# Kernel tuning notes

Hardware: AMD Instinct MI355X
Metric: run time of the kernel (lower is better)

Reference implementation:

```python
import jax, jax.numpy as jnp
from jax import lax
import numpy as np

H, W, C = 128, 128, 1024          # backbone feature map (stride-16, ResNet C4)
STRIDE = 16
NUM_ANCHORS = 9                   # 3 scales x 3 ratios
IOU_THRESHOLD = 0.7
SCORE_THRESHOLD = 0.5


def _make_anchors():
    scales = np.array([128.0, 256.0, 512.0], np.float32)
    ratios = np.array([0.5, 1.0, 2.0], np.float32)
    hs = (scales[:, None] * np.sqrt(ratios)[None, :]).reshape(-1)   # [9]
    ws = (scales[:, None] / np.sqrt(ratios)[None, :]).reshape(-1)   # [9]
    cy = (np.arange(H, dtype=np.float32) + 0.5) * STRIDE
    cx = (np.arange(W, dtype=np.float32) + 0.5) * STRIDE
    anc = np.zeros((H, W, NUM_ANCHORS, 4), np.float32)
    anc[..., 0] = cy[:, None, None]
    anc[..., 1] = cx[None, :, None]
    anc[..., 2] = hs
    anc[..., 3] = ws
    return anc.reshape(-1, 4)      # [N,4] as (cy, cx, h, w)


def _conv(x, w, b):
    return lax.conv_general_dilated(
        x, w, (1, 1), 'SAME', dimension_numbers=('NHWC', 'HWIO', 'NHWC')) + b


def _rpn_head(features, w1, b1, w2, b2, w_score, b_score, w_box, b_box):
    x = jax.nn.relu(features)
    x = _conv(x, w1, b1)
    x = jax.nn.relu(x)
    x = _conv(x, w2, b2)
    scores = jax.nn.sigmoid(_conv(x, w_score, b_score))   # [1,H,W,9]
    shifts = _conv(x, w_box, b_box)                        # [1,H,W,36]
    return scores.reshape(-1, 1), shifts.reshape(-1, 4)


def _decode(shifts, anchors):
    acy, acx, ah, aw = anchors[:, 0], anchors[:, 1], anchors[:, 2], anchors[:, 3]
    dy, dx, dh, dw = shifts[:, 0], shifts[:, 1], shifts[:, 2], shifts[:, 3]
    cy = acy + dy * ah
    cx = acx + dx * aw
    h = ah * jnp.exp(dh)
    w = aw * jnp.exp(dw)
    y1 = jnp.clip(cy - 0.5 * h, 0.0, H * STRIDE)
    x1 = jnp.clip(cx - 0.5 * w, 0.0, W * STRIDE)
    y2 = jnp.clip(cy + 0.5 * h, 0.0, H * STRIDE)
    x2 = jnp.clip(cx + 0.5 * w, 0.0, W * STRIDE)
    return jnp.stack([y1, x1, y2, x2], axis=-1)            # [N,4]


def _nms(boxes, scores, max_out):
    """Greedy NMS like tf.image.non_max_suppression, fixed-size padded output."""
    n = boxes.shape[0]
    areas = (boxes[:, 2] - boxes[:, 0]) * (boxes[:, 3] - boxes[:, 1])

    def body(state):
        suppressed, sel, count = state
        masked = jnp.where(suppressed, -jnp.inf, scores)
        i = jnp.argmax(masked)
        valid = masked[i] >= SCORE_THRESHOLD
        sel = sel.at[count].set(jnp.where(valid, i.astype(jnp.int32), -1))
        count = count + valid.astype(jnp.int32)
        b = boxes[i]
        iy = jnp.maximum(0.0, jnp.minimum(b[2], boxes[:, 2]) - jnp.maximum(b[0], boxes[:, 0]))
        ix = jnp.maximum(0.0, jnp.minimum(b[3], boxes[:, 3]) - jnp.maximum(b[1], boxes[:, 1]))
        inter = iy * ix
        iou = inter / (areas[i] + areas - inter + 1e-9)
        new_sup = (suppressed | (iou > IOU_THRESHOLD)).at[i].set(True)
        suppressed = jnp.where(valid, new_sup, jnp.ones_like(suppressed))
        return suppressed, sel, count

    def cond(state):
        suppressed, sel, count = state
        return (count < max_out) & (~jnp.all(suppressed))

    sel0 = jnp.full((max_out,), -1, jnp.int32)
    sup0 = jnp.zeros((n,), bool)
    _, sel, _ = lax.while_loop(cond, body, (sup0, sel0, jnp.int32(0)))
    valid = sel >= 0
    idx = jnp.where(valid, sel, 0)
    return boxes[idx] * valid[:, None], scores[idx] * valid, valid


def setup_inputs() -> dict:
    key = jax.random.key(0)
    ks = jax.random.split(key, 5)
    def init_w(k, shape, fan_in, scale=1.0):
        return jax.random.normal(k, shape, jnp.float32) * (scale / np.sqrt(fan_in))
    features = jax.random.normal(ks[0], (1, H, W, C), jnp.float32)
    w1 = init_w(ks[1], (3, 3, C, 512), 9 * C)
    b1 = jnp.zeros((512,), jnp.float32)
    w2 = init_w(ks[2], (3, 3, 512, 512), 9 * 512)
    b2 = jnp.zeros((512,), jnp.float32)
    w_score = init_w(ks[3], (1, 1, 512, NUM_ANCHORS), 512)
    b_score = jnp.zeros((NUM_ANCHORS,), jnp.float32)
    w_box = init_w(ks[4], (1, 1, 512, 4 * NUM_ANCHORS), 512, scale=0.1)
    b_box = jnp.zeros((4 * NUM_ANCHORS,), jnp.float32)
    return {"features": features, "w1": w1, "b1": b1, "w2": w2, "b2": b2,
            "w_score": w_score, "b_score": b_score,
            "w_box": w_box, "b_box": b_box, "region_limit": 300}


def reference(features, w1, b1, w2, b2, w_score, b_score, w_box, b_box, region_limit):
    pred_scores, pred_shifts = _rpn_head(features, w1, b1, w2, b2,
                                         w_score, b_score, w_box, b_box)
    anchors = jnp.asarray(_make_anchors())
    boxes = _decode(pred_shifts, anchors)
    return _nms(boxes, pred_scores[:, 0], int(region_limit))
```

## Files before the change

kernel.cpp:

```cpp
#include <hip/hip_runtime.h>

#define HW 128
#define COUTC 512
#define NB 4097
#define NSEL 300
#define T_TOP 4096
#define TW 64
#define FAST_N 1024

typedef _Float16 half8 __attribute__((ext_vector_type(8)));
typedef _Float16 half4v __attribute__((ext_vector_type(4)));
typedef float floatx4 __attribute__((ext_vector_type(4)));

#define NWS_A1H   ((size_t)0)
#define NWS_A1L   ((size_t)34611200)
#define NWS_W1H   ((size_t)69222400)
#define NWS_W1L   ((size_t)78659584)
#define NWS_A2H   ((size_t)88096768)
#define NWS_A2L   ((size_t)105402368)
#define NWS_W2H   ((size_t)122707968)
#define NWS_W2L   ((size_t)127426560)
#define NWS_X2    ((size_t)132145152)
#define NWS_BOXES ((size_t)165699584)
#define NWS_KEYS  ((size_t)168058880)
#define NWS_SKEYS ((size_t)169238528)
#define NWS_HIST  ((size_t)170418176)
#define NWS_CUR   ((size_t)170434816)
#define NWS_CNT   ((size_t)170451456)
#define NWS_BASE  ((size_t)170451712)
#define NWS_TOTAL ((size_t)170468352)

#define WS_X1     ((size_t)0)
#define WS_X2     ((size_t)33554432)
#define WS_BOXES  ((size_t)67108864)
#define WS_KEYS   ((size_t)69468160)
#define WS_SKEYS  ((size_t)70647808)
#define WS_HIST   ((size_t)71827456)
#define WS_CUR    ((size_t)71844096)
#define WS_CNT    ((size_t)71860736)
#define WS_BASE   ((size_t)71860992)

__device__ __forceinline__ void glds16(const void* g, void* l) {
    __builtin_amdgcn_global_load_lds(
        (const __attribute__((address_space(1))) void*)g,
        (__attribute__((address_space(3))) void*)l, 16, 0, 0);
}


__global__ __launch_bounds__(256) void convert_feat_kernel(
    const float* __restrict__ feat, _Float16* __restrict__ ah, _Float16* __restrict__ al)
{
    __shared__ __align__(16) _Float16 lh[130 * 32];
    __shared__ __align__(16) _Float16 ll[130 * 32];
    int pr = blockIdx.x;
    int chunk = blockIdx.y;
    int t = threadIdx.x;
    int c  = t & 31;
    int pg = t >> 5;
    bool interior = (pr >= 1 && pr <= 128);
    if (interior) {
        for (int px = pg; px < 128; px += 8) {
            float x = feat[((size_t)(pr - 1) * 128 + px) * 1024 + chunk * 32 + c];
            x = fmaxf(x, 0.f);
            _Float16 hi = (_Float16)x;
            lh[(px + 1) * 32 + c] = hi;
            ll[(px + 1) * 32 + c] = (_Float16)(x - (float)hi);
        }
    } else {
        for (int px = pg; px < 128; px += 8) {
            lh[(px + 1) * 32 + c] = (_Float16)0.f;
            ll[(px + 1) * 32 + c] = (_Float16)0.f;
        }
    }
    if (t < 32) {
        lh[t] = (_Float16)0.f;          ll[t] = (_Float16)0.f;
        lh[129 * 32 + t] = (_Float16)0.f; ll[129 * 32 + t] = (_Float16)0.f;
    }
    __syncthreads();
    size_t base = (size_t)pr * 133120 + (size_t)chunk * 4160;
    for (int i = t; i < 520; i += 256) {
        int sub = i / 130;
        int pc  = i - sub * 130;
        *(float4*)&ah[base + sub * 1040 + pc * 8] = *(const float4*)&lh[pc * 32 + sub * 8];
        *(float4*)&al[base + sub * 1040 + pc * 8] = *(const float4*)&ll[pc * 32 + sub * 8];
    }
}

template<int CIN>
__device__ __forceinline__ void convert_w_body(
    int b, const float* __restrict__ w, _Float16* __restrict__ wh, _Float16* __restrict__ wl)
{
    constexpr int NU = CIN / 8;
    int gid = b * 256 + threadIdx.x;
    int oc = gid & 511;
    int rest = gid >> 9;
    int u = rest & (NU - 1);
    int tap = rest / NU;
    if (tap >= 9) return;
    int k0 = u * 8;
    half8 vh, vl;
    #pragma unroll
    for (int j = 0; j < 8; ++j) {
        float v = w[((size_t)tap * CIN + k0 + j) * 512 + oc] * 64.f;
        _Float16 hi = (_Float16)v;
        vh[j] = hi;
        vl[j] = (_Float16)(v - (float)hi);
    }
    size_t o = (size_t)tap * CIN * 512 + (size_t)(k0 >> 5) * 16384
             + (size_t)((k0 >> 3) & 3) * 4096 + (size_t)oc * 8;
    *(half8*)(wh + o) = vh;
    *(half8*)(wl + o) = vl;
}

__global__ __launch_bounds__(256) void prep_kernel(
    const float* __restrict__ w1, _Float16* __restrict__ w1h, _Float16* __restrict__ w1l,
    const float* __restrict__ w2, _Float16* __restrict__ w2h, _Float16* __restrict__ w2l,
    const float* __restrict__ w_s, const float* __restrict__ w_b,
    _Float16* __restrict__ wbh, _Float16* __restrict__ wbl,
    _Float16* __restrict__ a2h, _Float16* __restrict__ a2l)
{
    int b = blockIdx.x;
    if (b < 2304) { convert_w_body<1024>(b, w1, w1h, w1l); return; }
    if (b < 3456) { convert_w_body<512>(b - 2304, w2, w2h, w2l); return; }
    if (b < 3584) {
        int gid = (b - 3456) * 256 + threadIdx.x;
        int n = gid & 63;
        int k = gid >> 6;
        float v = 0.f;
        if (n < 9)       v = w_s[k * 9 + n] * 64.f;
        else if (n < 45) v = w_b[k * 36 + (n - 9)] * 64.f;
        _Float16 hi = (_Float16)v;
        size_t o = (size_t)(k >> 5) * 2048 + (size_t)((k >> 3) & 3) * 512 + (size_t)n * 8 + (k & 7);
        wbh[o] = hi;
        wbl[o] = (_Float16)(v - (float)hi);
        return;
    }
    {
        int i = b - 3584;
        int pr, pc;
        if (i < 130)      { pr = 0;        pc = i; }
        else if (i < 260) { pr = 129;      pc = i - 130; }
        else if (i < 388) { pr = i - 259;  pc = 0; }
        else              { pr = i - 387;  pc = 129; }
        int t = threadIdx.x;
        if (t >= 128) return;
        _Float16* dst = (t & 64) ? a2l : a2h;
        int u = t & 63;
        size_t o = (size_t)pr * 66560 + (size_t)(u >> 2) * 4160 + (size_t)(u & 3) * 1040 + (size_t)pc * 8;
        *(float4*)(dst + o) = make_float4(0.f, 0.f, 0.f, 0.f);
    }
}

template<int CIN, bool PAD>
__global__ __launch_bounds__(256) void conv_mfma_kernel(
    const _Float16* __restrict__ ah, const _Float16* __restrict__ al,
    const _Float16* __restrict__ wh, const _Float16* __restrict__ wl,
    const float* __restrict__ bias,
    _Float16* __restrict__ oh, _Float16* __restrict__ ol)
{
    constexpr int ROWSTR = CIN * 130;
    constexpr int TAPW   = CIN * 512;
    __shared__ __align__(16) _Float16 lds[12288];

    int bx = blockIdx.x;
    int h  = bx & 127;
    int n0 = (bx >> 7) << 6;

    int tid  = threadIdx.x;
    int wave = tid >> 6;
    int lane = tid & 63;
    int fr = lane & 15;
    int fq = lane >> 4;

    int aoff0 = fq * 1040 + (32 * wave + fr) * 8;
    int aoff1 = aoff0 + 128;
    int boffB = fq * 4096 + (n0 + 32 * (wave & 1) + 16 * (wave >> 1) + fr) * 8;

    int wm = wave & 1, wn = wave >> 1;

    floatx4 acc[4][2];
    #pragma unroll
    for (int i = 0; i < 4; ++i)
        #pragma unroll
        for (int j = 0; j < 2; ++j)
            acc[i][j] = (floatx4){0.f, 0.f, 0.f, 0.f};

    _Float16* A0 = lds + wave * 1024;
    _Float16* L0 = lds + 4096 + wave * 1024;
    _Float16* B0 = lds + 8192 + (wave & 1) * 1024 + (wave >> 1) * 512;
    _Float16* C0 = B0 + 2048;

    const _Float16* rAh = lds + wm * 2048 + fq * 128 + fr * 8;
    const _Float16* rAl = rAh + 4096;
    const _Float16* rBh = lds + 8192 + wn * 1024 + fq * 128 + fr * 8;
    const _Float16* rBl = rBh + 2048;

    #pragma unroll
    for (int tap = 0; tap < 9; ++tap) {
        int dy = tap / 3 - 1, dx = tap % 3 - 1;
        const _Float16* gAh = ah + (size_t)(h + dy + 1) * ROWSTR + (dx + 1) * 8;
        const _Float16* gAl = al + (size_t)(h + dy + 1) * ROWSTR + (dx + 1) * 8;
        const _Float16* gBh = wh + (size_t)tap * TAPW;
        const _Float16* gBl = wl + (size_t)tap * TAPW;

        for (int kc = 0; kc < CIN; kc += 32) {
            int ab = (kc >> 5) * 4160;
            int bb = (kc >> 5) * 16384;
            glds16(gAh + ab + aoff0, A0);
            glds16(gAh + ab + aoff1, A0 + 512);
            glds16(gAl + ab + aoff0, L0);
            glds16(gAl + ab + aoff1, L0 + 512);
            glds16(gBh + bb + boffB, B0);
            glds16(gBl + bb + boffB, C0);
            __syncthreads();

            half8 fah[4], fal[4], fbh[2], fbl[2];
            #pragma unroll
            for (int i = 0; i < 4; ++i) {
                fah[i] = *(const half8*)(rAh + i * 512);
                fal[i] = *(const half8*)(rAl + i * 512);
            }
            #pragma unroll
            for (int j = 0; j < 2; ++j) {
                fbh[j] = *(const half8*)(rBh + j * 512);
                fbl[j] = *(const half8*)(rBl + j * 512);
            }
            #pragma unroll
            for (int i = 0; i < 4; ++i)
                #pragma unroll
                for (int j = 0; j < 2; ++j)
                    acc[i][j] = __builtin_amdgcn_mfma_f32_16x16x32_f16(fah[i], fbh[j], acc[i][j], 0, 0, 0);
            #pragma unroll
            for (int i = 0; i < 4; ++i)
                #pragma unroll
                for (int j = 0; j < 2; ++j)
                    acc[i][j] = __builtin_amdgcn_mfma_f32_16x16x32_f16(fah[i], fbl[j], acc[i][j], 0, 0, 0);
            #pragma unroll
            for (int i = 0; i < 4; ++i)
                #pragma unroll
                for (int j = 0; j < 2; ++j)
                    acc[i][j] = __builtin_amdgcn_mfma_f32_16x16x32_f16(fal[i], fbh[j], acc[i][j], 0, 0, 0);
            __syncthreads();
        }
    }

    const float scale = 1.f / 64.f;
    int em = 64 * wm + fq * 4;
    int en = 32 * wn + fr;
    #pragma unroll
    for (int j = 0; j < 2; ++j) {
        int oc = n0 + en + 16 * j;
        float b2 = bias[oc];
        #pragma unroll
        for (int i = 0; i < 4; ++i) {
            #pragma unroll
            for (int r = 0; r < 4; ++r) {
                int w = em + 16 * i + r;
                float v = fmaf(acc[i][j][r], scale, b2);
                if (PAD) {
                    v = fmaxf(v, 0.f);
                    _Float16 hi = (_Float16)v;
                    size_t o = (size_t)(h + 1) * 66560 + (size_t)(oc >> 5) * 4160
                             + (size_t)((oc >> 3) & 3) * 1040 + (size_t)(w + 1) * 8 + (oc & 7);
                    oh[o] = hi;
                    ol[o] = (_Float16)(v - (float)hi);
                } else {
                    _Float16 hi = (_Float16)v;
                    size_t o = (size_t)h * 65536 + (size_t)(oc >> 5) * 4096
                             + (size_t)((oc >> 3) & 3) * 1024 + (size_t)w * 8 + (oc & 7);
                    oh[o] = hi;
                    ol[o] = (_Float16)(v - (float)hi);
                }
            }
        }
    }
}

__device__ __forceinline__ void decode_emit(
    int gi, float z, float dyv, float dxv, float dhv, float dwv,
    float4* __restrict__ boxes, unsigned long long* __restrict__ keys,
    int* __restrict__ cnt, int* __restrict__ hist)
{
    int a = gi % 9;
    int pix = gi / 9;
    int h = pix >> 7, w = pix & 127;
    float sc  = (a < 3) ? 128.f : ((a < 6) ? 256.f : 512.f);
    int r = a - (a / 3) * 3;
    float ratio = (r == 0) ? 0.5f : ((r == 1) ? 1.f : 2.f);
    float sr = sqrtf(ratio);
    float ahh = sc * sr, aww = sc / sr;
    float acy = ((float)h + 0.5f) * 16.f;
    float acx = ((float)w + 0.5f) * 16.f;
    float cy = fmaf(dyv, ahh, acy);
    float cx = fmaf(dxv, aww, acx);
    float hh = ahh * expf(dhv);
    float ww = aww * expf(dwv);
    float y1 = fminf(fmaxf(cy - 0.5f * hh, 0.f), 2048.f);
    float x1 = fminf(fmaxf(cx - 0.5f * ww, 0.f), 2048.f);
    float y2 = fminf(fmaxf(cy + 0.5f * hh, 0.f), 2048.f);
    float x2 = fminf(fmaxf(cx + 0.5f * ww, 0.f), 2048.f);
    boxes[gi] = make_float4(y1, x1, y2, x2);
    float s = 1.f / (1.f + expf(-z));
    if (s >= 0.5f) {
        unsigned u = __float_as_uint(s);
        unsigned d = 0x3F800000u - u;
        unsigned long long key = ((unsigned long long)d << 18) | (unsigned)gi;
        int p = atomicAdd(cnt, 1);
        keys[p] = key;
        atomicAdd(&hist[d >> 11], 1);
    }
}

__global__ __launch_bounds__(256) void heads_mfma_kernel(
    const _Float16* __restrict__ xh, const _Float16* __restrict__ xl,
    const _Float16* __restrict__ wbh, const _Float16* __restrict__ wbl,
    const float* __restrict__ b_s, const float* __restrict__ b_b,
    float4* __restrict__ boxes, unsigned long long* __restrict__ keys,
    int* __restrict__ cnt, int* __restrict__ hist)
{
    __shared__ __align__(16) char smem[24576];
    _Float16* sAh = (_Float16*)smem;
    _Float16* sAl = (_Float16*)(smem + 8192);
    _Float16* sBh = (_Float16*)(smem + 16384);
    _Float16* sBl = (_Float16*)(smem + 20480);
    float* outs = (float*)smem;
    __shared__ float sb[48];

    int tid  = threadIdx.x;
    int wave = tid >> 6;
    int lane = tid & 63;
    int fr = lane & 15;
    int fq = lane >> 4;
    if (tid < 48) sb[tid] = (tid < 9) ? b_s[tid] : ((tid < 45) ? b_b[tid - 9] : 0.f);

    int h = blockIdx.x;
    int wm = wave & 1, wn = wave >> 1;

    floatx4 acc[4][2];
    #pragma unroll
    for (int i = 0; i < 4; ++i)
        #pragma unroll
        for (int j = 0; j < 2; ++j)
            acc[i][j] = (floatx4){0.f, 0.f, 0.f, 0.f};

    for (int kc = 0; kc < 16; ++kc) {
        const _Float16* gxh = xh + (size_t)h * 65536 + kc * 4096;
        const _Float16* gxl = xl + (size_t)h * 65536 + kc * 4096;
        glds16(gxh + tid * 8,        sAh + tid * 8);
        glds16(gxh + 2048 + tid * 8, sAh + 2048 + tid * 8);
        glds16(gxl + tid * 8,        sAl + tid * 8);
        glds16(gxl + 2048 + tid * 8, sAl + 2048 + tid * 8);
        glds16(wbh + kc * 2048 + tid * 8, sBh + tid * 8);
        glds16(wbl + kc * 2048 + tid * 8, sBl + tid * 8);
        __syncthreads();

        half8 fah[4], fal[4], fbh[2], fbl[2];
        #pragma unroll
        for (int i = 0; i < 4; ++i) {
            int px = wm * 64 + 16 * i + fr;
            int aaddr = fq * 1024 + px * 8;
            fah[i] = *(const half8*)(sAh + aaddr);
            fal[i] = *(const half8*)(sAl + aaddr);
        }
        #pragma unroll
        for (int j = 0; j < 2; ++j) {
            int n = wn * 32 + 16 * j + fr;
            int baddr = fq * 512 + n * 8;
            fbh[j] = *(const half8*)(sBh + baddr);
            fbl[j] = *(const half8*)(sBl + baddr);
        }
        #pragma unroll
        for (int i = 0; i < 4; ++i)
            #pragma unroll
            for (int j = 0; j < 2; ++j) {
                acc[i][j] = __builtin_amdgcn_mfma_f32_16x16x32_f16(fah[i], fbh[j], acc[i][j], 0, 0, 0);
                acc[i][j] = __builtin_amdgcn_mfma_f32_16x16x32_f16(fah[i], fbl[j], acc[i][j], 0, 0, 0);
                acc[i][j] = __builtin_amdgcn_mfma_f32_16x16x32_f16(fal[i], fbh[j], acc[i][j], 0, 0, 0);
            }
        __syncthreads();
    }

    const float scale = 1.f / 64.f;
    #pragma unroll
    for (int i = 0; i < 4; ++i)
        #pragma unroll
        for (int j = 0; j < 2; ++j)
            #pragma unroll
            for (int r = 0; r < 4; ++r) {
                int px = wm * 64 + 16 * i + fq * 4 + r;
                int n = wn * 32 + 16 * j + fr;
                if (n < 48)
                    outs[px * 48 + n] = fmaf(acc[i][j][r], scale, sb[n]);
            }
    __syncthreads();

    if (tid < 128) {
        int p = tid;
        #pragma unroll
        for (int a = 0; a < 9; ++a) {
            float z   = outs[p * 48 + a];
            float dyv = outs[p * 48 + 9 + 4 * a + 0];
            float dxv = outs[p * 48 + 9 + 4 * a + 1];
            float dhv = outs[p * 48 + 9 + 4 * a + 2];
            float dwv = outs[p * 48 + 9 + 4 * a + 3];
            int gi = (h * 128 + p) * 9 + a;
            decode_emit(gi, z, dyv, dxv, dhv, dwv, boxes, keys, cnt, hist);
        }
    }
}

template<int CIN, bool RELU_IN, bool RELU_OUT>
__global__ __launch_bounds__(256) void conv3x3_kernel(
    const float* __restrict__ in, const float* __restrict__ wgt,
    const float* __restrict__ bias, float* __restrict__ out)
{
    __shared__ float As[32][68];
    __shared__ float Bs[32][64];
    int bx = blockIdx.x;
    int mtile = bx & 255, ntile = bx >> 8;
    int h = mtile >> 1, w0 = (mtile & 1) << 6, n0 = ntile << 6;
    int tid = threadIdx.x, ty = tid >> 4, tx = tid & 15;
    float acc[4][4] = {{0.f}};
    const int KTOT = 9 * CIN;
    for (int k0 = 0; k0 < KTOT; k0 += 32) {
        int tap = k0 / CIN, icb = k0 % CIN;
        int dy = tap / 3 - 1, dx = tap % 3 - 1;
        int row = h + dy;
        bool rowok = ((unsigned)row < HW);
        {
            int pix = tid >> 3, cs = (tid & 7) << 2;
            #pragma unroll
            for (int p = 0; p < 2; ++p) {
                int px = pix + p * 32;
                int wcol = w0 + px + dx;
                float4 v = make_float4(0.f, 0.f, 0.f, 0.f);
                if (rowok && (unsigned)wcol < HW) {
                    v = *(const float4*)&in[((size_t)row * HW + wcol) * CIN + icb + cs];
                    if (RELU_IN) {
                        v.x = fmaxf(v.x, 0.f); v.y = fmaxf(v.y, 0.f);
                        v.z = fmaxf(v.z, 0.f); v.w = fmaxf(v.w, 0.f);
                    }
                }
                As[cs + 0][px] = v.x; As[cs + 1][px] = v.y;
                As[cs + 2][px] = v.z; As[cs + 3][px] = v.w;
            }
        }
        {
            int kr = tid >> 4, nc = (tid & 15) << 2;
            #pragma unroll
            for (int p = 0; p < 2; ++p) {
                int k = kr + p * 16;
                *(float4*)&Bs[k][nc] = *(const float4*)&wgt[(size_t)(k0 + k) * COUTC + n0 + nc];
            }
        }
        __syncthreads();
        #pragma unroll
        for (int kk = 0; kk < 32; ++kk) {
            float4 a = *(const float4*)&As[kk][ty << 2];
            float4 b = *(const float4*)&Bs[kk][tx << 2];
            float av[4] = {a.x, a.y, a.z, a.w};
            float bv[4] = {b.x, b.y, b.z, b.w};
            #pragma unroll
            for (int i = 0; i < 4; ++i)
                #pragma unroll
                for (int j = 0; j < 4; ++j)
                    acc[i][j] = fmaf(av[i], bv[j], acc[i][j]);
        }
        __syncthreads();
    }
    float4 bi = *(const float4*)&bias[n0 + (tx << 2)];
    float bv2[4] = {bi.x, bi.y, bi.z, bi.w};
    #pragma unroll
    for (int i = 0; i < 4; ++i) {
        float4 o;
        o.x = acc[i][0] + bv2[0]; o.y = acc[i][1] + bv2[1];
        o.z = acc[i][2] + bv2[2]; o.w = acc[i][3] + bv2[3];
        if (RELU_OUT) {
            o.x = fmaxf(o.x, 0.f); o.y = fmaxf(o.y, 0.f);
            o.z = fmaxf(o.z, 0.f); o.w = fmaxf(o.w, 0.f);
        }
        *(float4*)&out[((size_t)(h * HW) + w0 + (ty << 2) + i) * COUTC + n0 + (tx << 2)] = o;
    }
}

__global__ __launch_bounds__(256) void heads_decode_kernel(
    const float* __restrict__ x, const float* __restrict__ w_s, const float* __restrict__ b_s,
    const float* __restrict__ w_b, const float* __restrict__ b_b,
    float4* __restrict__ boxes, unsigned long long* __restrict__ keys,
    int* __restrict__ cnt, int* __restrict__ hist)
{
    __shared__ float xs[4][512];
    __shared__ float outs[4][45];
    int wave = threadIdx.x >> 6;
    int lane = threadIdx.x & 63;
    int pix  = blockIdx.x * 4 + wave;

    const float4* xp = (const float4*)&x[(size_t)pix * COUTC];
    *(float4*)&xs[wave][lane * 4]       = xp[lane];
    *(float4*)&xs[wave][256 + lane * 4] = xp[64 + lane];
    __syncthreads();

    if (lane < 45) {
        const float* wp; int stride; float acc;
        if (lane < 9) { wp = w_s + lane;       stride = 9;  acc = b_s[lane]; }
        else          { wp = w_b + (lane - 9); stride = 36; acc = b_b[lane - 9]; }
        const float* xrow = xs[wave];
        for (int k = 0; k < 512; k += 4) {
            acc = fmaf(xrow[k + 0], wp[(k + 0) * stride], acc);
            acc = fmaf(xrow[k + 1], wp[(k + 1) * stride], acc);
            acc = fmaf(xrow[k + 2], wp[(k + 2) * stride], acc);
            acc = fmaf(xrow[k + 3], wp[(k + 3) * stride], acc);
        }
        outs[wave][lane] = acc;
    }
    __syncthreads();

    if (lane < 9) {
        int a = lane;
        decode_emit(pix * 9 + a, outs[wave][a],
                    outs[wave][9 + 4 * a + 0], outs[wave][9 + 4 * a + 1],
                    outs[wave][9 + 4 * a + 2], outs[wave][9 + 4 * a + 3],
                    boxes, keys, cnt, hist);
    }
}

__global__ __launch_bounds__(256) void scan_kernel(
    const int* __restrict__ hist, int* __restrict__ base)
{
    __shared__ int tot[256];
    int t = threadIdx.x;
    int v[16];
    int s = 0;
    #pragma unroll
    for (int i = 0; i < 16; ++i) { v[i] = hist[t * 16 + i]; s += v[i]; }
    tot[t] = s;
    __syncthreads();
    for (int d = 1; d < 256; d <<= 1) {
        int x = (t >= d) ? tot[t - d] : 0;
        __syncthreads();
        tot[t] += x;
        __syncthreads();
    }
    int excl = (t == 0) ? 0 : tot[t - 1];
    #pragma unroll
    for (int i = 0; i < 16; ++i) { base[t * 16 + i] = excl; excl += v[i]; }
    if (t == 255) { base[4096] = excl; base[4097] = excl + hist[4096]; }
}

__global__ __launch_bounds__(256) void scatter_kernel(
    const unsigned long long* __restrict__ keys, const int* __restrict__ cnt,
    const int* __restrict__ base, int* __restrict__ cur,
    unsigned long long* __restrict__ skeys)
{
    int i = blockIdx.x * 256 + threadIdx.x;
    if (i < *cnt) {
        unsigned long long k = keys[i];
        int b = (int)(k >> 29);
        int p = base[b] + atomicAdd(&cur[b], 1);
        skeys[p] = k;
    }
}

__global__ __launch_bounds__(256) void sortb_kernel(
    const unsigned long long* __restrict__ skeys, const int* __restrict__ base,
    const float4* __restrict__ boxes,
    unsigned long long* __restrict__ sk2,
    float4* __restrict__ cboxes, float* __restrict__ careas)
{
    __shared__ unsigned long long sk[2048];
    int b = blockIdx.x;
    int s0 = base[b];
    int n = base[b + 1] - s0;
    if (n <= 0) return;
    int t = threadIdx.x;
    if (n <= 2048) {
        for (int i = t; i < n; i += 256) sk[i] = skeys[s0 + i];
        __syncthreads();
        for (int i = t; i < n; i += 256) {
            unsigned long long k = sk[i];
            int r = 0;
            for (int j = 0; j < n; ++j) r += (sk[j] < k) ? 1 : 0;
            int pos = s0 + r;
            sk2[pos] = k;
            if (pos < T_TOP) {
                float4 bb = boxes[k & 0x3FFFFull];
                cboxes[pos] = bb;
                careas[pos] = (bb.z - bb.x) * (bb.w - bb.y);
            }
        }
    } else {
        const unsigned long long* src = skeys + s0;
        for (int i = t; i < n; i += 256) {
            unsigned long long k = src[i];
            int r = 0;
            for (int j = 0; j < n; ++j) r += (src[j] < k) ? 1 : 0;
            int pos = s0 + r;
            sk2[pos] = k;
            if (pos < T_TOP) {
                float4 bb = boxes[k & 0x3FFFFull];
                cboxes[pos] = bb;
                careas[pos] = (bb.z - bb.x) * (bb.w - bb.y);
            }
        }
    }
}

__global__ __launch_bounds__(256) void mask_kernel(
    const float4* __restrict__ cboxes, const float* __restrict__ careas,
    unsigned long long* __restrict__ msk)
{
    int bi = blockIdx.y, bj = blockIdx.x;
    if (bj < bi) return;
    __shared__ float4 jb[256];
    __shared__ float  ja[256];
    int t = threadIdx.x;
    int j0 = bj << 8;
    jb[t] = cboxes[j0 + t];
    ja[t] = careas[j0 + t];
    __syncthreads();
    int i = (bi << 8) + t;
    float4 ci = cboxes[i];
    float ca = careas[i];
    unsigned long long word = 0;
    for (int jj = 0; jj < 256; ++jj) {
        int j = j0 + jj;
        float4 b = jb[jj];
        float iy = fmaxf(0.f, fminf(ci.z, b.z) - fmaxf(ci.x, b.x));
        float ix = fmaxf(0.f, fminf(ci.w, b.w) - fmaxf(ci.y, b.y));
        float inter = iy * ix;
        float iou = inter / (ca + ja[jj] - inter + 1e-9f);
        bool bit = (j == i) || (j > i && iou > 0.7f);
        if (bit) word |= 1ull << (jj & 63);
        if ((jj & 63) == 63) {
            msk[(size_t)i * TW + (bj << 2) + (jj >> 6)] = word;
            word = 0;
        }
    }
}

__global__ __launch_bounds__(256) void walk_kernel(
    const unsigned long long* __restrict__ sk2, const int* __restrict__ cnt,
    const float4* __restrict__ cboxes, const float* __restrict__ careas,
    const unsigned long long* __restrict__ msk, const float4* __restrict__ boxes,
    float* __restrict__ out)
{
    __shared__ unsigned long long mlds[FAST_N * 16];
    __shared__ unsigned long long sup[TW];
    __shared__ float4 sbox[NSEL];
    __shared__ float  sarea[NSEL];
    __shared__ unsigned short sellist[NSEL];
    int tid = threadIdx.x;
    for (int i = tid; i < 1800; i += 256) out[i] = 0.f;
    int total = *cnt;
    int Tc = min(total, T_TOP);
    int FN = min(Tc, FAST_N);
    for (int i = tid; i < FN * 16; i += 256) {
        mlds[i] = msk[(size_t)(i >> 4) * TW + (i & 15)];
    }
    if (tid < TW) sup[tid] = 0ull;
    __syncthreads();
    if (tid >= 64) return;
    int lane = tid;
    int sel = 0;

    {
        int p = 0;
        while (sel < NSEL) {
            int w0 = p >> 6;
            unsigned long long m = 0;
            if (lane < 16 && lane >= w0) {
                m = ~sup[lane];
                if (lane == w0) m &= (~0ull << (p & 63));
            }
            unsigned long long bal = __ballot(m != 0ull);
            if (bal == 0ull) break;
            int w = __builtin_ctzll(bal);
            int bit = __shfl(m ? __builtin_ctzll(m) : 0, w);
            int c = (w << 6) + bit;
            if (c >= FN) break;
            float4 cb = cboxes[c];
            float ca = careas[c];
            if (lane == 0) {
                unsigned long long key = sk2[c];
                out[sel * 4 + 0] = cb.x; out[sel * 4 + 1] = cb.y;
                out[sel * 4 + 2] = cb.z; out[sel * 4 + 3] = cb.w;
                out[1200 + sel] = __uint_as_float(0x3F800000u - (unsigned)(key >> 18));
                out[1500 + sel] = 1.f;
                sbox[sel] = cb;
                sarea[sel] = ca;
                sellist[sel] = (unsigned short)c;
            }
            sel++;
            if (lane < 16) sup[lane] |= mlds[c * 16 + lane];
            p = c + 1;
        }
    }

    if (sel < NSEL && Tc > FN) {
        unsigned long long acc = 0ull;
        if (lane >= 16) {
            for (int s = 0; s < sel; ++s)
                acc |= msk[(size_t)sellist[s] * TW + lane];
            sup[lane] = acc;
        }

        auto scanFrom = [&](int p) -> int {
            if (p < 0 || p >= Tc) return -1;
            int w = p >> 6;
            unsigned long long f = (~sup[w]) & (~0ull << (p & 63));
            while (f == 0ull) {
                ++w;
                if (w >= TW) return -1;
                f = ~sup[w];
            }
            int c = (w << 6) + __builtin_ctzll(f);
            return (c < Tc) ? c : -1;
        };

        unsigned long long r0 = 0, r1 = 0, r2n = 0;
        int idx = scanFrom(FN);
        if (idx >= 0) r0 = msk[(size_t)idx * TW + lane];
        int idx2 = (idx >= 0) ? scanFrom(idx + 1) : -1;
        if (idx2 >= 0) r1 = msk[(size_t)idx2 * TW + lane];

        while (idx >= 0 && sel < NSEL) {
            float4 cb = cboxes[idx];
            float ca = careas[idx];
            if (lane == 0) {
                unsigned long long key = sk2[idx];
                out[sel * 4 + 0] = cb.x; out[sel * 4 + 1] = cb.y;
                out[sel * 4 + 2] = cb.z; out[sel * 4 + 3] = cb.w;
                out[1200 + sel] = __uint_as_float(0x3F800000u - (unsigned)(key >> 18));
                out[1500 + sel] = 1.f;
                sbox[sel] = cb;
                sarea[sel] = ca;
            }
            sel++;
            if (sel >= NSEL) break;

            int idx3 = (idx2 >= 0) ? scanFrom(idx2 + 1) : -1;
            if (idx3 >= 0) r2n = msk[(size_t)idx3 * TW + lane];

            sup[lane] |= r0;

            if (idx2 >= 0) {
                unsigned long long w = sup[idx2 >> 6];
                if ((w >> (idx2 & 63)) & 1ull) {
                    idx2 = scanFrom(idx2);
                    if (idx2 >= 0) r1 = msk[(size_t)idx2 * TW + lane];
                    idx3 = (idx2 >= 0) ? scanFrom(idx2 + 1) : -1;
                    if (idx3 >= 0) r2n = msk[(size_t)idx3 * TW + lane];
                }
            }
            idx = idx2; r0 = r1;
            idx2 = idx3; r1 = r2n;
        }
    }

    if (sel < NSEL && total > T_TOP) {
        for (int i = T_TOP; i < total && sel < NSEL; ++i) {
            unsigned long long key = sk2[i];
            float4 cb = boxes[key & 0x3FFFFull];
            float ca = (cb.z - cb.x) * (cb.w - cb.y);
            int supp = 0;
            for (int t = lane; t < sel; t += 64) {
                float4 s4 = sbox[t];
                float iy = fmaxf(0.f, fminf(s4.z, cb.z) - fmaxf(s4.x, cb.x));
                float ix = fmaxf(0.f, fminf(s4.w, cb.w) - fmaxf(s4.y, cb.y));
                float inter = iy * ix;
                float iou = inter / (sarea[t] + ca - inter + 1e-9f);
                if (iou > 0.7f) supp = 1;
            }
            if (__ballot(supp) == 0ull) {
                if (lane == 0) {
                    out[sel * 4 + 0] = cb.x; out[sel * 4 + 1] = cb.y;
                    out[sel * 4 + 2] = cb.z; out[sel * 4 + 3] = cb.w;
                    out[1200 + sel] = __uint_as_float(0x3F800000u - (unsigned)(key >> 18));
                    out[1500 + sel] = 1.f;
                    sbox[sel] = cb;
                    sarea[sel] = ca;
                }
                sel++;
            }
        }
    }
}

extern "C" void kernel_launch(void* const* d_in, const int* in_sizes, int n_in,
                              void* d_out, int out_size, void* d_ws, size_t ws_size,
                              hipStream_t stream) {
    const float* feat = (const float*)d_in[0];
    const float* w1   = (const float*)d_in[1];
    const float* b1   = (const float*)d_in[2];
    const float* w2   = (const float*)d_in[3];
    const float* b2   = (const float*)d_in[4];
    const float* w_s  = (const float*)d_in[5];
    const float* b_s  = (const float*)d_in[6];
    const float* w_b  = (const float*)d_in[7];
    const float* b_b  = (const float*)d_in[8];
    float* out = (float*)d_out;
    char* ws = (char*)d_ws;

    if (ws_size >= NWS_TOTAL) {
        _Float16* a1h = (_Float16*)(ws + NWS_A1H);
        _Float16* a1l = (_Float16*)(ws + NWS_A1L);
        _Float16* w1h = (_Float16*)(ws + NWS_W1H);
        _Float16* w1l = (_Float16*)(ws + NWS_W1L);
        _Float16* a2h = (_Float16*)(ws + NWS_A2H);
        _Float16* a2l = (_Float16*)(ws + NWS_A2L);
        _Float16* w2h = (_Float16*)(ws + NWS_W2H);
        _Float16* w2l = (_Float16*)(ws + NWS_W2L);
        _Float16* xh  = (_Float16*)(ws + NWS_X2);
        _Float16* xl  = (_Float16*)(ws + NWS_X2 + 16777216);
        float4* boxes = (float4*)(ws + NWS_BOXES);
        unsigned long long* keys  = (unsigned long long*)(ws + NWS_KEYS);
        unsigned long long* skeys = (unsigned long long*)(ws + NWS_SKEYS);
        int* hist = (int*)(ws + NWS_HIST);
        int* cur  = (int*)(ws + NWS_CUR);
        int* cnt  = (int*)(ws + NWS_CNT);
        int* base = (int*)(ws + NWS_BASE);
        _Float16* wbh = (_Float16*)(ws + NWS_SKEYS);
        _Float16* wbl = (_Float16*)(ws + NWS_SKEYS + 65536);
        unsigned long long* msk = (unsigned long long*)(ws + NWS_A1H);
        float4* cbox  = (float4*)(ws + NWS_A1L);
        float*  carea = (float*)(ws + NWS_A1L + 262144);
        unsigned long long* sk2 = keys;

        hipMemsetAsync(ws + NWS_HIST, 0, (NWS_CNT - NWS_HIST) + 256, stream);
        convert_feat_kernel<<<dim3(130, 32), 256, 0, stream>>>(feat, a1h, a1l);
        prep_kernel<<<4100, 256, 0, stream>>>(w1, w1h, w1l, w2, w2h, w2l,
                                              w_s, w_b, wbh, wbl, a2h, a2l);
        conv_mfma_kernel<1024, true ><<<1024, 256, 0, stream>>>(a1h, a1l, w1h, w1l, b1, a2h, a2l);
        conv_mfma_kernel< 512, false><<<1024, 256, 0, stream>>>(a2h, a2l, w2h, w2l, b2, xh, xl);
        heads_mfma_kernel<<<128, 256, 0, stream>>>(xh, xl, wbh, wbl, b_s, b_b, boxes, keys, cnt, hist);
        scan_kernel<<<1, 256, 0, stream>>>(hist, base);
        scatter_kernel<<<576, 256, 0, stream>>>(keys, cnt, base, cur, skeys);
        sortb_kernel<<<NB, 256, 0, stream>>>(skeys, base, boxes, sk2, cbox, carea);
        mask_kernel<<<dim3(16, 16), 256, 0, stream>>>(cbox, carea, msk);
        walk_kernel<<<1, 256, 0, stream>>>(sk2, cnt, cbox, carea, msk, boxes, out);
    } else {
        float* x1 = (float*)(ws + WS_X1);
        float* x2 = (float*)(ws + WS_X2);
        float4* boxes = (float4*)(ws + WS_BOXES);
        unsigned long long* keys  = (unsigned long long*)(ws + WS_KEYS);
        unsigned long long* skeys = (unsigned long long*)(ws + WS_SKEYS);
        int* hist = (int*)(ws + WS_HIST);
        int* cur  = (int*)(ws + WS_CUR);
        int* cnt  = (int*)(ws + WS_CNT);
        int* base = (int*)(ws + WS_BASE);
        unsigned long long* msk = (unsigned long long*)(ws + WS_X1);
        float4* cbox  = (float4*)(ws + WS_X2);
        float*  carea = (float*)(ws + WS_X2 + 262144);
        unsigned long long* sk2 = keys;

        hipMemsetAsync(ws + WS_HIST, 0, (WS_CNT - WS_HIST) + 256, stream);
        conv3x3_kernel<1024, true,  true ><<<2048, 256, 0, stream>>>(feat, w1, b1, x1);
        conv3x3_kernel< 512, false, false><<<2048, 256, 0, stream>>>(x1,   w2, b2, x2);
        heads_decode_kernel<<<4096, 256, 0, stream>>>(x2, w_s, b_s, w_b, b_b, boxes, keys, cnt, hist);
        scan_kernel<<<1, 256, 0, stream>>>(hist, base);
        scatter_kernel<<<576, 256, 0, stream>>>(keys, cnt, base, cur, skeys);
        sortb_kernel<<<NB, 256, 0, stream>>>(skeys, base, boxes, sk2, cbox, carea);
        mask_kernel<<<dim3(16, 16), 256, 0, stream>>>(cbox, carea, msk);
        walk_kernel<<<1, 256, 0, stream>>>(sk2, cnt, cbox, carea, msk, boxes, out);
    }
}
```

Baseline: 998.7 us.

## Enlarge conv MFMA tile to 128x128 with 8 waves and 64-wide K steps

The two 3x3 conv kernels now run 512-thread blocks covering 128 output channels instead of 64, with eight waves each computing a 64x32 sub-tile. Each block stages two 32-channel K slabs per barrier pair, so it does half as many __syncthreads and reuses each activation tile across twice as many output channels. The cost is a 64 KB LDS footprint per block and a tighter launch-bounds register budget, which may lower occupancy or cause spills.

```diff
diff --git a/kernel.cpp b/kernel.cpp
--- a/kernel.cpp
+++ b/kernel.cpp
@@ -152,7 +152,7 @@
 }
 
 template<int CIN, bool PAD>
-__global__ __launch_bounds__(256) void conv_mfma_kernel(
+__global__ __launch_bounds__(512, 4) void conv_mfma_kernel(
     const _Float16* __restrict__ ah, const _Float16* __restrict__ al,
     const _Float16* __restrict__ wh, const _Float16* __restrict__ wl,
     const float* __restrict__ bias,
@@ -160,11 +160,11 @@
 {
     constexpr int ROWSTR = CIN * 130;
     constexpr int TAPW   = CIN * 512;
-    __shared__ __align__(16) _Float16 lds[12288];
+    __shared__ __align__(16) _Float16 lds[32768];
 
     int bx = blockIdx.x;
     int h  = bx & 127;
-    int n0 = (bx >> 7) << 6;
+    int n0 = (bx >> 7) << 7;
 
     int tid  = threadIdx.x;
     int wave = tid >> 6;
@@ -172,9 +172,8 @@
     int fr = lane & 15;
     int fq = lane >> 4;
 
-    int aoff0 = fq * 1040 + (32 * wave + fr) * 8;
-    int aoff1 = aoff0 + 128;
-    int boffB = fq * 4096 + (n0 + 32 * (wave & 1) + 16 * (wave >> 1) + fr) * 8;
+    int aoff0 = fq * 1040 + (16 * wave + fr) * 8;
+    int boff0 = fq * 4096 + (n0 + 16 * wave + fr) * 8;
 
     int wm = wave & 1, wn = wave >> 1;
 
@@ -184,16 +183,6 @@
         #pragma unroll
         for (int j = 0; j < 2; ++j)
             acc[i][j] = (floatx4){0.f, 0.f, 0.f, 0.f};
-
-    _Float16* A0 = lds + wave * 1024;
-    _Float16* L0 = lds + 4096 + wave * 1024;
-    _Float16* B0 = lds + 8192 + (wave & 1) * 1024 + (wave >> 1) * 512;
-    _Float16* C0 = B0 + 2048;
-
-    const _Float16* rAh = lds + wm * 2048 + fq * 128 + fr * 8;
-    const _Float16* rAl = rAh + 4096;
-    const _Float16* rBh = lds + 8192 + wn * 1024 + fq * 128 + fr * 8;
-    const _Float16* rBl = rBh + 2048;
 
     #pragma unroll
     for (int tap = 0; tap < 9; ++tap) {
@@ -203,43 +192,56 @@
         const _Float16* gBh = wh + (size_t)tap * TAPW;
         const _Float16* gBl = wl + (size_t)tap * TAPW;
 
-        for (int kc = 0; kc < CIN; kc += 32) {
-            int ab = (kc >> 5) * 4160;
-            int bb = (kc >> 5) * 16384;
-            glds16(gAh + ab + aoff0, A0);
-            glds16(gAh + ab + aoff1, A0 + 512);
-            glds16(gAl + ab + aoff0, L0);
-            glds16(gAl + ab + aoff1, L0 + 512);
-            glds16(gBh + bb + boffB, B0);
-            glds16(gBl + bb + boffB, C0);
+        for (int kc = 0; kc < CIN; kc += 64) {
+            #pragma unroll
+            for (int s = 0; s < 2; ++s) {
+                int ab = ((kc >> 5) + s) * 4160;
+                int bb = ((kc >> 5) + s) * 16384;
+                _Float16* dA = lds +          s * 4096 + wave * 512;
+                _Float16* dL = lds + 8192  +  s * 4096 + wave * 512;
+                _Float16* dB = lds + 16384 +  s * 4096 + wave * 512;
+                _Float16* dC = lds + 24576 +  s * 4096 + wave * 512;
+                glds16(gAh + ab + aoff0, dA);
+                glds16(gAl + ab + aoff0, dL);
+                glds16(gBh + bb + boff0, dB);
+                glds16(gBl + bb + boff0, dC);
+            }
             __syncthreads();
 
-            half8 fah[4], fal[4], fbh[2], fbl[2];
             #pragma unroll
-            for (int i = 0; i < 4; ++i) {
-                fah[i] = *(const half8*)(rAh + i * 512);
-                fal[i] = *(const half8*)(rAl + i * 512);
-            }
-            #pragma unroll
-            for (int j = 0; j < 2; ++j) {
-                fbh[j] = *(const half8*)(rBh + j * 512);
-                fbl[j] = *(const half8*)(rBl + j * 512);
-            }
-            #pragma unroll
-            for (int i = 0; i < 4; ++i)
+            for (int s = 0; s < 2; ++s) {
+                const _Float16* rAh = lds +          s * 4096 + wm * 2048 + fq * 128 + fr * 8;
+                const _Float16* rAl = rAh + 8192;
+                const _Float16* rBh = lds + 16384 +  s * 4096 + wn * 1024 + fq * 128 + fr * 8;
+                const _Float16* rBl = rBh + 8192;
+
+                half8 fah[4], fal[4], fbh[2], fbl[2];
                 #pragma unroll
-                for (int j = 0; j < 2; ++j)
-                    acc[i][j] = __builtin_amdgcn_mfma_f32_16x16x32_f16(fah[i], fbh[j], acc[i][j], 0, 0, 0);
-            #pragma unroll
-            for (int i = 0; i < 4; ++i)
+                for (int i = 0; i < 4; ++i) {
+                    fah[i] = *(const half8*)(rAh + i * 512);
+                    fal[i] = *(const half8*)(rAl + i * 512);
+                }
                 #pragma unroll
-                for (int j = 0; j < 2; ++j)
-                    acc[i][j] = __builtin_amdgcn_mfma_f32_16x16x32_f16(fah[i], fbl[j], acc[i][j], 0, 0, 0);
-            #pragma unroll
-            for (int i = 0; i < 4; ++i)
+                for (int j = 0; j < 2; ++j) {
+                    fbh[j] = *(const half8*)(rBh + j * 512);
+                    fbl[j] = *(const half8*)(rBl + j * 512);
+                }
                 #pragma unroll
-                for (int j = 0; j < 2; ++j)
-                    acc[i][j] = __builtin_amdgcn_mfma_f32_16x16x32_f16(fal[i], fbh[j], acc[i][j], 0, 0, 0);
+                for (int i = 0; i < 4; ++i)
+                    #pragma unroll
+                    for (int j = 0; j < 2; ++j)
+                        acc[i][j] = __builtin_amdgcn_mfma_f32_16x16x32_f16(fah[i], fbh[j], acc[i][j], 0, 0, 0);
+                #pragma unroll
+                for (int i = 0; i < 4; ++i)
+                    #pragma unroll
+                    for (int j = 0; j < 2; ++j)
+                        acc[i][j] = __builtin_amdgcn_mfma_f32_16x16x32_f16(fah[i], fbl[j], acc[i][j], 0, 0, 0);
+                #pragma unroll
+                for (int i = 0; i < 4; ++i)
+                    #pragma unroll
+                    for (int j = 0; j < 2; ++j)
+                        acc[i][j] = __builtin_amdgcn_mfma_f32_16x16x32_f16(fal[i], fbh[j], acc[i][j], 0, 0, 0);
+            }
             __syncthreads();
         }
     }
@@ -830,8 +832,8 @@
         convert_feat_kernel<<<dim3(130, 32), 256, 0, stream>>>(feat, a1h, a1l);
         prep_kernel<<<4100, 256, 0, stream>>>(w1, w1h, w1l, w2, w2h, w2l,
                                               w_s, w_b, wbh, wbl, a2h, a2l);
-        conv_mfma_kernel<1024, true ><<<1024, 256, 0, stream>>>(a1h, a1l, w1h, w1l, b1, a2h, a2l);
-        conv_mfma_kernel< 512, false><<<1024, 256, 0, stream>>>(a2h, a2l, w2h, w2l, b2, xh, xl);
+        conv_mfma_kernel<1024, true ><<<512, 512, 0, stream>>>(a1h, a1l, w1h, w1l, b1, a2h, a2l);
+        conv_mfma_kernel< 512, false><<<512, 512, 0, stream>>>(a2h, a2l, w2h, w2l, b2, xh, xl);
         heads_mfma_kernel<<<128, 256, 0, stream>>>(xh, xl, wbh, wbl, b_s, b_b, boxes, keys, cnt, hist);
         scan_kernel<<<1, 256, 0, stream>>>(hist, base);
         scatter_kernel<<<576, 256, 0, stream>>>(keys, cnt, base, cur, skeys);
```

New measurement: 891.4 us. 1.12x faster.
